# Performance work log

Hardware: AMD Instinct MI355X
Metric: run time of the kernel (lower is better)

Reference implementation:

```python
import jax, jax.numpy as jnp
import numpy as np

B, N, E = 2, 2048, 2048
HQ, HKV, D = 32, 8, 64
SCALE = 1.0 / np.sqrt(D)


def setup_inputs() -> dict:
    key = jax.random.key(0)
    ks = jax.random.split(key, 9)
    s = lambda k, shape, fan: jax.random.normal(k, shape, jnp.float32) / np.sqrt(fan)
    return {
        "x": jax.random.normal(ks[0], (B, N, E), jnp.float32),
        "Wq": s(ks[1], (HQ * D, E), E),
        "bq": jnp.zeros((HQ * D,), jnp.float32),
        "Wk": s(ks[2], (HKV * D, E), E),
        "bk": jnp.zeros((HKV * D,), jnp.float32),
        "Wv": s(ks[3], (HKV * D, E), E),
        "bv": jnp.zeros((HKV * D,), jnp.float32),
        "Wo": s(ks[4], (E, E), E),
        "bo": jnp.zeros((E,), jnp.float32),
    }


def _attention(x, Wq, bq, Wk, bk, Wv, bv, Wo, bo):
    G = HQ // HKV  # query heads per kv head
    # projections (torch Linear: y = x @ W.T + b)
    q = (jnp.einsum("bne,fe->bnf", x, Wq) + bq).reshape(B, N, HKV, G, D)
    k = (jnp.einsum("bne,fe->bnf", x, Wk) + bk).reshape(B, N, HKV, D)
    v = (jnp.einsum("bne,fe->bnf", x, Wv) + bv).reshape(B, N, HKV, D)
    # scores [B, HKV, G, N, N] -- GQA without materializing repeated K/V
    scores = jnp.einsum("bnhgd,bmhd->bhgnm", q, k) * SCALE
    causal = jnp.tril(jnp.ones((N, N), bool))
    scores = jnp.where(causal, scores, -jnp.inf)
    p = jax.nn.softmax(scores, axis=-1)
    o = jnp.einsum("bhgnm,bmhd->bnhgd", p, v).reshape(B, N, E)
    return jnp.einsum("bne,fe->bnf", o, Wo) + bo


def reference(x, Wq, bq, Wk, bk, Wv, bv, Wo, bo):
    return _attention(x, Wq, bq, Wk, bk, Wv, bv, Wo, bo)
```

## Files before the change

### kernel.cpp

```cpp
#include <hip/hip_runtime.h>
#include <hip/hip_bf16.h>


#define B_   2
#define N_   2048
#define E_   2048
#define HQ_  32
#define HKV_ 8
#define D_   64
#define BN_  (B_*N_)

typedef __attribute__((ext_vector_type(8))) short bf16x8;
typedef __attribute__((ext_vector_type(4))) float f32x4;

#define MFMA16(a,b,c) __builtin_amdgcn_mfma_f32_16x16x32_bf16(a,b,c,0,0,0)

__device__ inline unsigned short f2bf(float f) {
  unsigned u = __builtin_bit_cast(unsigned, f);
  u += 0x7FFFu + ((u >> 16) & 1u);
  return (unsigned short)(u >> 16);
}

__device__ inline void gload_lds16(const void* g, void* l) {
  __builtin_amdgcn_global_load_lds(
      (const __attribute__((address_space(1))) void*)g,
      (__attribute__((address_space(3))) void*)l, 16, 0, 0);
}

__global__ void cast_all(const float* __restrict__ x,  const float* __restrict__ wq,
                         const float* __restrict__ wk, const float* __restrict__ wv,
                         const float* __restrict__ wo, unsigned short* __restrict__ dst) {
  const int c0 = 2097152;
  const int c1 = c0 + 1048576;
  const int c2 = c1 + 262144;
  const int c3 = c2 + 262144;
  const int c4 = c3 + 1048576;
  int i = blockIdx.x * blockDim.x + threadIdx.x;
  const int stride = gridDim.x * blockDim.x;
  for (; i < c4; i += stride) {
    const float* src; int off;
    if      (i < c0) { src = x;  off = i; }
    else if (i < c1) { src = wq; off = i - c0; }
    else if (i < c2) { src = wk; off = i - c1; }
    else if (i < c3) { src = wv; off = i - c2; }
    else             { src = wo; off = i - c3; }
    float4 f = reinterpret_cast<const float4*>(src)[off];
    ushort4 u;
    u.x = f2bf(f.x); u.y = f2bf(f.y); u.z = f2bf(f.z); u.w = f2bf(f.w);
    reinterpret_cast<ushort4*>(dst)[i] = u;
  }
}

__global__ __launch_bounds__(512) void gemm_qkv(
    const unsigned short* __restrict__ A,
    const unsigned short* __restrict__ Wq, const unsigned short* __restrict__ Wk,
    const unsigned short* __restrict__ Wv,
    const float* __restrict__ bq, const float* __restrict__ bk, const float* __restrict__ bv,
    unsigned short* __restrict__ Qo, unsigned short* __restrict__ Ko,
    unsigned short* __restrict__ Vto)
{
  __shared__ __align__(16) unsigned short As[2][2][8192];
  __shared__ __align__(16) unsigned short Bs[2][2][8192];
  const int tid  = threadIdx.x;
  const int lane = tid & 63;
  const int w    = tid >> 6;
  const int g    = blockIdx.x & 7;
  const int s    = blockIdx.x >> 3;
  const int bm   = g*2 + (s >= 12);
  const int bn   = (s >= 12) ? (s - 12) : s;
  const int m0   = bm << 8;
  const int n0v  = bn << 8;
  const int K    = E_;

  const unsigned short* W; const float* bias; int wn0, seg;
  if      (n0v < 2048) { W = Wq; bias = bq; wn0 = n0v;        seg = 0; }
  else if (n0v < 2560) { W = Wk; bias = bk; wn0 = n0v - 2048; seg = 1; }
  else                 { W = Wv; bias = bv; wn0 = n0v - 2560; seg = 2; }

  const int mr   = w >> 2;
  const int nc   = w & 3;
  const int cl   = lane & 15;
  const int kgrp = lane >> 4;
  const int rl   = kgrp << 2;

  const int srow = tid >> 2;
  const unsigned sch = ((unsigned)((tid & 3) ^ (srow & 3))) << 3;
  const unsigned short* gAb = A + (size_t)(m0  + srow) * K + sch;
  const unsigned short* gBb = W + (size_t)(wn0 + srow) * K + sch;
  const unsigned ldse = (unsigned)tid * 8u;

  const unsigned rch = ((unsigned)(kgrp ^ (cl & 3))) << 3;
  unsigned rAo[2][4], rBo[4];
  #pragma unroll
  for (int mq = 0; mq < 2; ++mq)
    #pragma unroll
    for (int z = 0; z < 4; ++z)
      rAo[mq][z] = (unsigned)(mr*128 + mq*64 + z*16 + cl) * 32u + rch;
  #pragma unroll
  for (int jj = 0; jj < 4; ++jj)
    rBo[jj] = (unsigned)(nc*64 + jj*16 + cl) * 32u + rch;

  f32x4 acc[8][4] = {};
  const int nt = K >> 6;

  auto STAGE = [&](int kt, int buf, int kh) {
    const int ko = (kt << 6) + (kh << 5);
    #pragma unroll
    for (int q = 0; q < 2; ++q)
      gload_lds16(gAb + (size_t)(q*128)*K + ko, &As[buf][kh][ldse + q*4096u]);
    #pragma unroll
    for (int q = 0; q < 2; ++q)
      gload_lds16(gBb + (size_t)(q*128)*K + ko, &Bs[buf][kh][ldse + q*4096u]);
  };

  STAGE(0, 0, 0);
  STAGE(0, 0, 1);

  for (int t = 0; t < nt; ++t) {
    const int p = t & 1;
    #pragma unroll
    for (int ks = 0; ks < 2; ++ks) {
      if (t + 1 < nt) {
        STAGE(t + 1, p ^ 1, ks);
        asm volatile("s_waitcnt vmcnt(8)" ::: "memory");
      } else if (ks == 0) {
        asm volatile("s_waitcnt vmcnt(4)" ::: "memory");
      } else {
        asm volatile("s_waitcnt vmcnt(0)" ::: "memory");
      }
      __builtin_amdgcn_s_barrier();
      const unsigned short* Ah = As[p][ks];
      const unsigned short* Bh = Bs[p][ks];
      bf16x8 bfr[4];
      #pragma unroll
      for (int jj = 0; jj < 4; ++jj)
        bfr[jj] = *reinterpret_cast<const bf16x8*>(&Bh[rBo[jj]]);
      #pragma unroll
      for (int mq = 0; mq < 2; ++mq) {
        bf16x8 af[4];
        #pragma unroll
        for (int z = 0; z < 4; ++z)
          af[z] = *reinterpret_cast<const bf16x8*>(&Ah[rAo[mq][z]]);
        __builtin_amdgcn_s_setprio(1);
        #pragma unroll
        for (int z = 0; z < 4; ++z)
          #pragma unroll
          for (int jj = 0; jj < 4; ++jj)
            acc[mq*4 + z][jj] = MFMA16(af[z], bfr[jj], acc[mq*4 + z][jj]);
        __builtin_amdgcn_s_setprio(0);
      }
    }
  }

  #pragma unroll
  for (int mi = 0; mi < 8; ++mi) {
    const int rowb = m0 + mr*128 + (mi >> 2)*64 + (mi & 3)*16 + rl;
    #pragma unroll
    for (int jj = 0; jj < 4; ++jj) {
      const int col = wn0 + nc*64 + jj*16 + cl;
      const float bj = bias[col];
      if (seg == 0) {
        #pragma unroll
        for (int r = 0; r < 4; ++r)
          Qo[(size_t)(rowb + r) * 2048 + col] = f2bf(acc[mi][jj][r] + bj);
      } else if (seg == 1) {
        #pragma unroll
        for (int r = 0; r < 4; ++r)
          Ko[(size_t)(rowb + r) * 512 + col] = f2bf(acc[mi][jj][r] + bj);
      } else {
        ushort4 u;
        u.x = f2bf(acc[mi][jj][0] + bj);
        u.y = f2bf(acc[mi][jj][1] + bj);
        u.z = f2bf(acc[mi][jj][2] + bj);
        u.w = f2bf(acc[mi][jj][3] + bj);
        *reinterpret_cast<ushort4*>(&Vto[(size_t)col * 4096 + rowb]) = u;
      }
    }
  }
}

__global__ __launch_bounds__(256) void gemm_out(
    const unsigned short* __restrict__ A, const unsigned short* __restrict__ W,
    const float* __restrict__ bias, float* __restrict__ C)
{
  __shared__ __align__(16) unsigned short As[128*64];
  __shared__ __align__(16) unsigned short Bs[128*64];
  const int tid  = threadIdx.x;
  const int w    = tid >> 6;
  const int lane = tid & 63;
  const int bm   = blockIdx.x >> 4;
  const int bn   = blockIdx.x & 15;
  const int m0   = bm << 7, n0 = bn << 7;
  const int K    = E_;
  const int wr   = (w >> 1) << 6;
  const int wc   = (w & 1) << 6;
  const int cl   = lane & 15;
  const int kgrp = lane >> 4;
  const int rl   = kgrp << 2;
  const int li   = lane >> 3;
  const int lx   = lane & 7;

  const unsigned schunk = ((unsigned)(lx ^ li)) << 3;
  const unsigned short* gA = A + (size_t)(m0 + li) * K + schunk;
  const unsigned short* gB = W + (size_t)(n0 + li) * K + schunk;
  unsigned short* lA = As + lane*8;
  unsigned short* lB = Bs + lane*8;

  unsigned rA[4][2], rB[4][2];
  #pragma unroll
  for (int z = 0; z < 4; ++z)
    #pragma unroll
    for (int ks = 0; ks < 2; ++ks) {
      rA[z][ks] = (unsigned)(wr + z*16 + cl)*64u + ((((unsigned)ks*4u + (unsigned)kgrp) ^ (unsigned)(cl & 7)) << 3);
      rB[z][ks] = (unsigned)(wc + z*16 + cl)*64u + ((((unsigned)ks*4u + (unsigned)kgrp) ^ (unsigned)(cl & 7)) << 3);
    }

  f32x4 acc[4][4] = {};

  for (int kt = 0; kt < (K >> 6); ++kt) {
    const int ko = kt << 6;
    #pragma unroll
    for (int q = 0; q < 4; ++q) {
      const unsigned i = (unsigned)(w*4 + q);
      gload_lds16(gA + ((size_t)i*8*K + ko), lA + i*512);
      gload_lds16(gB + ((size_t)i*8*K + ko), lB + i*512);
    }
    __syncthreads();
    #pragma unroll
    for (int ks = 0; ks < 2; ++ks) {
      bf16x8 af[4], bfr[4];
      #pragma unroll
      for (int i = 0; i < 4; ++i)
        af[i] = *reinterpret_cast<const bf16x8*>(&As[rA[i][ks]]);
      #pragma unroll
      for (int j = 0; j < 4; ++j)
        bfr[j] = *reinterpret_cast<const bf16x8*>(&Bs[rB[j][ks]]);
      #pragma unroll
      for (int i = 0; i < 4; ++i)
        #pragma unroll
        for (int j = 0; j < 4; ++j)
          acc[i][j] = MFMA16(af[i], bfr[j], acc[i][j]);
    }
    __syncthreads();
  }

  #pragma unroll
  for (int j = 0; j < 4; ++j) {
    const int col = n0 + wc + j*16 + cl;
    const float bj = bias[col];
    #pragma unroll
    for (int i = 0; i < 4; ++i) {
      const int row = m0 + wr + i*16 + rl;
      #pragma unroll
      for (int r = 0; r < 4; ++r)
        C[(size_t)(row + r) * E_ + col] = acc[i][j][r] + bj;
    }
  }
}

__global__ __launch_bounds__(256, 2) void attn_kernel(
    const unsigned short* __restrict__ Q, const unsigned short* __restrict__ K,
    const unsigned short* __restrict__ Vt, unsigned short* __restrict__ O)
{
  __shared__ __align__(16) unsigned short Kbuf[2][4096];
  __shared__ __align__(16) unsigned short Vbuf[2][4096];
  __shared__ __align__(16) unsigned short Ps[4][2048];
  const int tid  = threadIdx.x;
  const int w    = tid >> 6;
  const int lane = tid & 63;
  const int bh   = blockIdx.x;
  const int b    = bh >> 3;
  const int h    = bh & 7;
  const int j    = blockIdx.y;
  const int hq   = h*4 + w;
  const int cl   = lane & 15;
  const int kgrp = lane >> 4;
  const int rl   = kgrp << 2;
  const int li   = lane >> 3;
  const int lx   = lane & 7;

  const float K2 = 0.125f * 1.44269504088896340736f;

  char* pws = (char*)&Ps[w][0];
  const unsigned swz = ((unsigned)(cl & 7)) << 4;

  bf16x8 ones8;
  #pragma unroll
  for (int q = 0; q < 8; ++q) ones8[q] = (short)0x3F80;

  const char* Kp = (const char*)(K + (size_t)(b*N_)*512 + h*64);
  const char* Vp = (const char*)(Vt + (size_t)(h*64)*BN_ + b*N_);

  const unsigned schunk = ((unsigned)(lx ^ li)) << 4;
  const unsigned kso  = (unsigned)li*1024u + schunk;
  const unsigned vso  = (unsigned)li*8192u + schunk;
  const unsigned ldst = (unsigned)lane*16u;

  unsigned rdo[4][2];
  #pragma unroll
  for (int z = 0; z < 4; ++z)
    #pragma unroll
    for (int ks = 0; ks < 2; ++ks)
      rdo[z][ks] = (unsigned)z*2048u + (unsigned)cl*128u
                 + ((((unsigned)ks*4u + (unsigned)kgrp) ^ (unsigned)(cl & 7)) << 4);

  unsigned wb[2][4], rb[2][2];
  #pragma unroll
  for (int i = 0; i < 2; ++i) {
    #pragma unroll
    for (int c = 0; c < 4; ++c)
      wb[i][c] = (unsigned)i*2048u + (unsigned)cl*128u
               + (((unsigned)c*32u + (unsigned)kgrp*8u) ^ swz);
    #pragma unroll
    for (int ks = 0; ks < 2; ++ks)
      rb[i][ks] = (unsigned)i*2048u + (unsigned)cl*128u
                + (((unsigned)ks*64u + (unsigned)kgrp*16u) ^ swz);
  }

  for (int sp = 0; sp < 2; ++sp) {
    __syncthreads();
    const int sidx = sp ? (63 - j) : j;
    const int q0   = sidx << 5;
    const int nt   = (sidx >> 1) + 1;

    bf16x8 qf[2][2];
    #pragma unroll
    for (int i = 0; i < 2; ++i) {
      const size_t qoff = (size_t)(b*N_ + q0 + i*16 + cl) * E_ + hq*64 + (kgrp << 3);
      qf[i][0] = *reinterpret_cast<const bf16x8*>(Q + qoff);
      qf[i][1] = *reinterpret_cast<const bf16x8*>(Q + qoff + 32);
    }

    f32x4 o[2][4] = {};
    f32x4 l4[2] = {};
    float m[2] = {-1e30f, -1e30f};

    #pragma unroll
    for (int q = 0; q < 2; ++q) {
      const unsigned i = (unsigned)(w*2 + q);
      gload_lds16(Kp + (i*8192u + kso),  (char*)Kbuf[0] + (i*1024u + ldst));
      gload_lds16(Vp + (i*65536u + vso), (char*)Vbuf[0] + (i*1024u + ldst));
    }
    int cur = 0;
    __syncthreads();

    for (int t = 0; t < nt; ++t) {
      if (t + 1 < nt) {
        const unsigned kt = (unsigned)(t + 1) * 65536u;
        const unsigned vt = (unsigned)(t + 1) * 128u;
        #pragma unroll
        for (int q = 0; q < 2; ++q) {
          const unsigned i = (unsigned)(w*2 + q);
          gload_lds16(Kp + (kt + i*8192u + kso),  (char*)Kbuf[cur^1] + (i*1024u + ldst));
          gload_lds16(Vp + (vt + i*65536u + vso), (char*)Vbuf[cur^1] + (i*1024u + ldst));
        }
      }

      bf16x8 kf[4][2];
      #pragma unroll
      for (int c = 0; c < 4; ++c)
        #pragma unroll
        for (int ks = 0; ks < 2; ++ks)
          kf[c][ks] = *reinterpret_cast<const bf16x8*>((const char*)Kbuf[cur] + rdo[c][ks]);

      f32x4 s[2][4];
      #pragma unroll
      for (int i = 0; i < 2; ++i)
        #pragma unroll
        for (int c = 0; c < 4; ++c) {
          f32x4 z = {};
          z = MFMA16(kf[c][0], qf[i][0], z);
          z = MFMA16(kf[c][1], qf[i][1], z);
          s[i][c] = z;
        }

      if (t == nt - 1) {
        const int kvb = t << 6;
        #pragma unroll
        for (int i = 0; i < 2; ++i) {
          const int qq = q0 + i*16 + cl;
          #pragma unroll
          for (int c = 0; c < 4; ++c)
            #pragma unroll
            for (int r = 0; r < 4; ++r)
              if (kvb + c*16 + rl + r > qq) s[i][c][r] = -1e30f;
        }
      }

      #pragma unroll
      for (int i = 0; i < 2; ++i) {
        float t0 = fmaxf(fmaxf(s[i][0][0], s[i][0][1]), fmaxf(s[i][0][2], s[i][0][3]));
        float t1 = fmaxf(fmaxf(s[i][1][0], s[i][1][1]), fmaxf(s[i][1][2], s[i][1][3]));
        float t2 = fmaxf(fmaxf(s[i][2][0], s[i][2][1]), fmaxf(s[i][2][2], s[i][2][3]));
        float t3 = fmaxf(fmaxf(s[i][3][0], s[i][3][1]), fmaxf(s[i][3][2], s[i][3][3]));
        float tm = fmaxf(fmaxf(t0, t1), fmaxf(t2, t3));
        tm = fmaxf(tm, __shfl_xor(tm, 16, 64));
        tm = fmaxf(tm, __shfl_xor(tm, 32, 64));
        const float mn = fmaxf(m[i], tm);
        const float al = __builtin_amdgcn_exp2f(K2 * (m[i] - mn));
        m[i] = mn;
        l4[i] *= al;
        #pragma unroll
        for (int db = 0; db < 4; ++db) o[i][db] *= al;
        #pragma unroll
        for (int c = 0; c < 4; ++c) {
          ushort4 u;
          u.x = f2bf(__builtin_amdgcn_exp2f(K2 * (s[i][c][0] - mn)));
          u.y = f2bf(__builtin_amdgcn_exp2f(K2 * (s[i][c][1] - mn)));
          u.z = f2bf(__builtin_amdgcn_exp2f(K2 * (s[i][c][2] - mn)));
          u.w = f2bf(__builtin_amdgcn_exp2f(K2 * (s[i][c][3] - mn)));
          *reinterpret_cast<ushort4*>(pws + wb[i][c]) = u;
        }
      }

      bf16x8 vf[4][2];
      #pragma unroll
      for (int db = 0; db < 4; ++db)
        #pragma unroll
        for (int ks = 0; ks < 2; ++ks)
          vf[db][ks] = *reinterpret_cast<const bf16x8*>((const char*)Vbuf[cur] + rdo[db][ks]);

      #pragma unroll
      for (int i = 0; i < 2; ++i) {
        const bf16x8 pa0 = *reinterpret_cast<const bf16x8*>(pws + rb[i][0]);
        const bf16x8 pa1 = *reinterpret_cast<const bf16x8*>(pws + rb[i][1]);
        l4[i] = MFMA16(ones8, pa0, l4[i]);
        l4[i] = MFMA16(ones8, pa1, l4[i]);
        #pragma unroll
        for (int db = 0; db < 4; ++db) {
          o[i][db] = MFMA16(vf[db][0], pa0, o[i][db]);
          o[i][db] = MFMA16(vf[db][1], pa1, o[i][db]);
        }
      }

      __syncthreads();
      cur ^= 1;
    }

    #pragma unroll
    for (int i = 0; i < 2; ++i) {
      const float inv = 1.0f / l4[i][0];
      const size_t orow = (size_t)(b*N_ + q0 + i*16 + cl) * E_ + hq*64 + rl;
      #pragma unroll
      for (int db = 0; db < 4; ++db) {
        ushort4 u;
        u.x = f2bf(o[i][db][0] * inv);
        u.y = f2bf(o[i][db][1] * inv);
        u.z = f2bf(o[i][db][2] * inv);
        u.w = f2bf(o[i][db][3] * inv);
        *reinterpret_cast<ushort4*>(&O[orow + db*16]) = u;
      }
    }
  }
}

extern "C" void kernel_launch(void* const* d_in, const int* in_sizes, int n_in,
                              void* d_out, int out_size, void* d_ws, size_t ws_size,
                              hipStream_t stream) {
  const float* x  = (const float*)d_in[0];
  const float* Wq = (const float*)d_in[1];
  const float* bq = (const float*)d_in[2];
  const float* Wk = (const float*)d_in[3];
  const float* bk = (const float*)d_in[4];
  const float* Wv = (const float*)d_in[5];
  const float* bv = (const float*)d_in[6];
  const float* Wo = (const float*)d_in[7];
  const float* bo = (const float*)d_in[8];
  float* out = (float*)d_out;

  unsigned short* ws  = (unsigned short*)d_ws;
  unsigned short* xb  = ws;
  unsigned short* Wqb = xb  + 8388608;
  unsigned short* Wkb = Wqb + 4194304;
  unsigned short* Wvb = Wkb + 1048576;
  unsigned short* Wob = Wvb + 1048576;
  unsigned short* Qb  = Wob + 4194304;
  unsigned short* Kb  = Qb  + 8388608;
  unsigned short* Vtb = Kb  + 2097152;
  unsigned short* Ob  = Vtb + 2097152;

  cast_all<<<dim3(2048), dim3(256), 0, stream>>>(x, Wq, Wk, Wv, Wo, xb);

  gemm_qkv<<<dim3(192), dim3(512), 0, stream>>>(xb, Wqb, Wkb, Wvb,
                                                bq, bk, bv, Qb, Kb, Vtb);

  attn_kernel<<<dim3(16, 32), dim3(256), 0, stream>>>(Qb, Kb, Vtb, Ob);

  gemm_out<<<dim3(32*16), dim3(256), 0, stream>>>(Ob, Wob, bo, out);
}
```

Before: 196.6 us.

## Retile QKV GEMM to 128x192 tiles with 512 blocks and occupancy hint

Changes the fused QKV projection GEMM from 256x256 tiles on 192 blocks to 128x192 tiles on 512 blocks, so that tiles can straddle the Q/K/V weight boundaries and the grid covers the 256 CUs more evenly. It uses a single 64-wide K stage per buffer with an 8-chunk XOR swizzle, a 5-load prefetch wait and a second barrier per iteration, and adds a launch_bounds occupancy hint of 4. The smaller tiles reduce register and LDS pressure and fix the wave-quantization tail, at the cost of lower arithmetic intensity per block and an extra synchronization per k-step.

```diff
diff --git a/kernel.cpp b/kernel.cpp
--- a/kernel.cpp
+++ b/kernel.cpp
@@ -51,7 +51,7 @@
   }
 }
 
-__global__ __launch_bounds__(512) void gemm_qkv(
+__global__ __launch_bounds__(512, 4) void gemm_qkv(
     const unsigned short* __restrict__ A,
     const unsigned short* __restrict__ Wq, const unsigned short* __restrict__ Wk,
     const unsigned short* __restrict__ Wv,
@@ -59,120 +59,125 @@
     unsigned short* __restrict__ Qo, unsigned short* __restrict__ Ko,
     unsigned short* __restrict__ Vto)
 {
-  __shared__ __align__(16) unsigned short As[2][2][8192];
-  __shared__ __align__(16) unsigned short Bs[2][2][8192];
+  __shared__ __align__(16) unsigned short As[2][8192];
+  __shared__ __align__(16) unsigned short Bs[2][12288];
   const int tid  = threadIdx.x;
+  const int w    = tid >> 6;
   const int lane = tid & 63;
-  const int w    = tid >> 6;
   const int g    = blockIdx.x & 7;
   const int s    = blockIdx.x >> 3;
-  const int bm   = g*2 + (s >= 12);
-  const int bn   = (s >= 12) ? (s - 12) : s;
-  const int m0   = bm << 8;
-  const int n0v  = bn << 8;
+  const int bm   = g*4 + (s >> 4);
+  const int bn   = s & 15;
+  const int m0   = bm << 7;
+  const int n0v  = bn * 192;
   const int K    = E_;
 
-  const unsigned short* W; const float* bias; int wn0, seg;
-  if      (n0v < 2048) { W = Wq; bias = bq; wn0 = n0v;        seg = 0; }
-  else if (n0v < 2560) { W = Wk; bias = bk; wn0 = n0v - 2048; seg = 1; }
-  else                 { W = Wv; bias = bv; wn0 = n0v - 2560; seg = 2; }
-
-  const int mr   = w >> 2;
-  const int nc   = w & 3;
+  const int mgrp = w >> 2;
+  const int ngrp = w & 3;
   const int cl   = lane & 15;
   const int kgrp = lane >> 4;
   const int rl   = kgrp << 2;
-
-  const int srow = tid >> 2;
-  const unsigned sch = ((unsigned)((tid & 3) ^ (srow & 3))) << 3;
-  const unsigned short* gAb = A + (size_t)(m0  + srow) * K + sch;
-  const unsigned short* gBb = W + (size_t)(wn0 + srow) * K + sch;
-  const unsigned ldse = (unsigned)tid * 8u;
-
-  const unsigned rch = ((unsigned)(kgrp ^ (cl & 3))) << 3;
-  unsigned rAo[2][4], rBo[4];
-  #pragma unroll
-  for (int mq = 0; mq < 2; ++mq)
+  const int li   = lane >> 3;
+  const int lx   = lane & 7;
+
+  const unsigned gsw = ((unsigned)(lx ^ li)) << 3;
+  const unsigned short* gA = A + (size_t)(m0 + w*16 + li) * K + gsw;
+  const unsigned short* gBq[3];
+  #pragma unroll
+  for (int q = 0; q < 3; ++q) {
+    const int vr = n0v + w*24 + q*8;
+    const unsigned short* base;
+    if (vr < 2048)      base = Wq + (size_t)vr * K;
+    else if (vr < 2560) base = Wk + (size_t)(vr - 2048) * K;
+    else                base = Wv + (size_t)(vr - 2560) * K;
+    gBq[q] = base + (size_t)li * K + gsw;
+  }
+  const unsigned aDst = (unsigned)(w*16)*64u + (unsigned)lane*8u;
+  const unsigned bDst = (unsigned)(w*24)*64u + (unsigned)lane*8u;
+
+  unsigned rAo[4][2], rBo[3][2];
+  #pragma unroll
+  for (int ks = 0; ks < 2; ++ks) {
+    const unsigned c8 = (((unsigned)(ks*4 + kgrp)) ^ (unsigned)(cl & 7)) << 3;
     #pragma unroll
     for (int z = 0; z < 4; ++z)
-      rAo[mq][z] = (unsigned)(mr*128 + mq*64 + z*16 + cl) * 32u + rch;
-  #pragma unroll
-  for (int jj = 0; jj < 4; ++jj)
-    rBo[jj] = (unsigned)(nc*64 + jj*16 + cl) * 32u + rch;
-
-  f32x4 acc[8][4] = {};
+      rAo[z][ks] = (unsigned)(mgrp*64 + z*16 + cl) * 64u + c8;
+    #pragma unroll
+    for (int jj = 0; jj < 3; ++jj)
+      rBo[jj][ks] = (unsigned)(ngrp*48 + jj*16 + cl) * 64u + c8;
+  }
+
+  f32x4 acc[4][3] = {};
   const int nt = K >> 6;
 
-  auto STAGE = [&](int kt, int buf, int kh) {
-    const int ko = (kt << 6) + (kh << 5);
+  auto STAGE = [&](int kt, int buf) {
+    const int ko = kt << 6;
     #pragma unroll
     for (int q = 0; q < 2; ++q)
-      gload_lds16(gAb + (size_t)(q*128)*K + ko, &As[buf][kh][ldse + q*4096u]);
-    #pragma unroll
-    for (int q = 0; q < 2; ++q)
-      gload_lds16(gBb + (size_t)(q*128)*K + ko, &Bs[buf][kh][ldse + q*4096u]);
+      gload_lds16(gA + (size_t)(q*8)*K + ko, &As[buf][aDst + q*512u]);
+    #pragma unroll
+    for (int q = 0; q < 3; ++q)
+      gload_lds16(gBq[q] + ko, &Bs[buf][bDst + q*512u]);
   };
 
-  STAGE(0, 0, 0);
-  STAGE(0, 0, 1);
+  STAGE(0, 0);
+  int p = 0;
 
   for (int t = 0; t < nt; ++t) {
-    const int p = t & 1;
+    if (t + 1 < nt) {
+      STAGE(t + 1, p ^ 1);
+      asm volatile("s_waitcnt vmcnt(5)" ::: "memory");
+    } else {
+      asm volatile("s_waitcnt vmcnt(0)" ::: "memory");
+    }
+    __builtin_amdgcn_s_barrier();
     #pragma unroll
     for (int ks = 0; ks < 2; ++ks) {
-      if (t + 1 < nt) {
-        STAGE(t + 1, p ^ 1, ks);
-        asm volatile("s_waitcnt vmcnt(8)" ::: "memory");
-      } else if (ks == 0) {
-        asm volatile("s_waitcnt vmcnt(4)" ::: "memory");
+      bf16x8 af[4], bfr[3];
+      #pragma unroll
+      for (int z = 0; z < 4; ++z)
+        af[z] = *reinterpret_cast<const bf16x8*>(&As[p][rAo[z][ks]]);
+      #pragma unroll
+      for (int jj = 0; jj < 3; ++jj)
+        bfr[jj] = *reinterpret_cast<const bf16x8*>(&Bs[p][rBo[jj][ks]]);
+      __builtin_amdgcn_s_setprio(1);
+      #pragma unroll
+      for (int z = 0; z < 4; ++z)
+        #pragma unroll
+        for (int jj = 0; jj < 3; ++jj)
+          acc[z][jj] = MFMA16(af[z], bfr[jj], acc[z][jj]);
+      __builtin_amdgcn_s_setprio(0);
+    }
+    __builtin_amdgcn_s_barrier();
+    p ^= 1;
+  }
+
+  #pragma unroll
+  for (int z = 0; z < 4; ++z) {
+    const int rowb = m0 + mgrp*64 + z*16 + rl;
+    #pragma unroll
+    for (int jj = 0; jj < 3; ++jj) {
+      const int col16 = n0v + ngrp*48 + jj*16;
+      if (col16 < 2048) {
+        const int col = col16 + cl;
+        const float bj = bq[col];
+        #pragma unroll
+        for (int r = 0; r < 4; ++r)
+          Qo[(size_t)(rowb + r) * 2048 + col] = f2bf(acc[z][jj][r] + bj);
+      } else if (col16 < 2560) {
+        const int col = col16 - 2048 + cl;
+        const float bj = bk[col];
+        #pragma unroll
+        for (int r = 0; r < 4; ++r)
+          Ko[(size_t)(rowb + r) * 512 + col] = f2bf(acc[z][jj][r] + bj);
       } else {
-        asm volatile("s_waitcnt vmcnt(0)" ::: "memory");
-      }
-      __builtin_amdgcn_s_barrier();
-      const unsigned short* Ah = As[p][ks];
-      const unsigned short* Bh = Bs[p][ks];
-      bf16x8 bfr[4];
-      #pragma unroll
-      for (int jj = 0; jj < 4; ++jj)
-        bfr[jj] = *reinterpret_cast<const bf16x8*>(&Bh[rBo[jj]]);
-      #pragma unroll
-      for (int mq = 0; mq < 2; ++mq) {
-        bf16x8 af[4];
-        #pragma unroll
-        for (int z = 0; z < 4; ++z)
-          af[z] = *reinterpret_cast<const bf16x8*>(&Ah[rAo[mq][z]]);
-        __builtin_amdgcn_s_setprio(1);
-        #pragma unroll
-        for (int z = 0; z < 4; ++z)
-          #pragma unroll
-          for (int jj = 0; jj < 4; ++jj)
-            acc[mq*4 + z][jj] = MFMA16(af[z], bfr[jj], acc[mq*4 + z][jj]);
-        __builtin_amdgcn_s_setprio(0);
-      }
-    }
-  }
-
-  #pragma unroll
-  for (int mi = 0; mi < 8; ++mi) {
-    const int rowb = m0 + mr*128 + (mi >> 2)*64 + (mi & 3)*16 + rl;
-    #pragma unroll
-    for (int jj = 0; jj < 4; ++jj) {
-      const int col = wn0 + nc*64 + jj*16 + cl;
-      const float bj = bias[col];
-      if (seg == 0) {
-        #pragma unroll
-        for (int r = 0; r < 4; ++r)
-          Qo[(size_t)(rowb + r) * 2048 + col] = f2bf(acc[mi][jj][r] + bj);
-      } else if (seg == 1) {
-        #pragma unroll
-        for (int r = 0; r < 4; ++r)
-          Ko[(size_t)(rowb + r) * 512 + col] = f2bf(acc[mi][jj][r] + bj);
-      } else {
+        const int col = col16 - 2560 + cl;
+        const float bj = bv[col];
         ushort4 u;
-        u.x = f2bf(acc[mi][jj][0] + bj);
-        u.y = f2bf(acc[mi][jj][1] + bj);
-        u.z = f2bf(acc[mi][jj][2] + bj);
-        u.w = f2bf(acc[mi][jj][3] + bj);
+        u.x = f2bf(acc[z][jj][0] + bj);
+        u.y = f2bf(acc[z][jj][1] + bj);
+        u.z = f2bf(acc[z][jj][2] + bj);
+        u.w = f2bf(acc[z][jj][3] + bj);
         *reinterpret_cast<ushort4*>(&Vto[(size_t)col * 4096 + rowb]) = u;
       }
     }
@@ -481,7 +486,7 @@
 
   cast_all<<<dim3(2048), dim3(256), 0, stream>>>(x, Wq, Wk, Wv, Wo, xb);
 
-  gemm_qkv<<<dim3(192), dim3(512), 0, stream>>>(xb, Wqb, Wkb, Wvb,
+  gemm_qkv<<<dim3(512), dim3(512), 0, stream>>>(xb, Wqb, Wkb, Wvb,
                                                 bq, bk, bv, Qb, Kb, Vtb);
 
   attn_kernel<<<dim3(16, 32), dim3(256), 0, stream>>>(Qb, Kb, Vtb, Ob);
```

Measured after the change: 182.0 us. 7.4% less time.
